# Performance work log

Measured on AMD Instinct MI355X. Metric: run time of the kernel, lower is better.

## Reference

```python
import jax, jax.numpy as jnp
import numpy as np

C = 256
NUM_HEADS = 4
NBLK = 6  # 3 stages x depth 2
WS = (2, 8, 8)   # 3D window
SS = (1, 4, 4)   # shift for odd blocks
N_WIN = WS[0] * WS[1] * WS[2]  # 128 tokens per window
RPB_SIZE = (2 * WS[0] - 1) * (2 * WS[1] - 1) * (2 * WS[2] - 1)  # 675


def _rel_index():
    coords = np.stack(np.meshgrid(np.arange(WS[0]), np.arange(WS[1]), np.arange(WS[2]), indexing='ij'))
    coords = coords.reshape(3, -1)
    rel = (coords[:, :, None] - coords[:, None, :]).transpose(1, 2, 0)
    rel[:, :, 0] += WS[0] - 1
    rel[:, :, 1] += WS[1] - 1
    rel[:, :, 2] += WS[2] - 1
    rel[:, :, 0] *= (2 * WS[1] - 1) * (2 * WS[2] - 1)
    rel[:, :, 1] *= (2 * WS[2] - 1)
    return jnp.asarray(rel.sum(-1))  # [N_WIN, N_WIN]

REL_IDX = _rel_index()


def window_partition(x):
    # [B,D,H,W,C] -> [B*nW, N_WIN, C]
    B, D, H, W, Cc = x.shape
    x = x.reshape(B, D // WS[0], WS[0], H // WS[1], WS[1], W // WS[2], WS[2], Cc)
    return x.transpose(0, 1, 3, 5, 2, 4, 6, 7).reshape(-1, N_WIN, Cc)


def window_reverse(win, B, D, H, W):
    Cc = win.shape[-1]
    x = win.reshape(B, D // WS[0], H // WS[1], W // WS[2], WS[0], WS[1], WS[2], Cc)
    return x.transpose(0, 1, 4, 2, 5, 3, 6, 7).reshape(B, D, H, W, Cc)


def attn_mask(D, H, W):
    # standard shifted-window mask, computed on host constants
    img = np.zeros((1, D, H, W, 1), np.float32)
    cnt = 0
    for d in (slice(0, -WS[0]), slice(-WS[0], -SS[0]), slice(-SS[0], None)):
        for h in (slice(0, -WS[1]), slice(-WS[1], -SS[1]), slice(-SS[1], None)):
            for w in (slice(0, -WS[2]), slice(-WS[2], -SS[2]), slice(-SS[2], None)):
                img[:, d, h, w, :] = cnt
                cnt += 1
    mw = img.reshape(1, D // WS[0], WS[0], H // WS[1], WS[1], W // WS[2], WS[2], 1)
    mw = mw.transpose(0, 1, 3, 5, 2, 4, 6, 7).reshape(-1, N_WIN)
    diff = mw[:, None, :] - mw[:, :, None]
    return jnp.asarray(np.where(diff != 0, -100.0, 0.0).astype(np.float32))  # [nW,N,N]


def layer_norm(x, g, b):
    mu = x.mean(-1, keepdims=True)
    var = ((x - mu) ** 2).mean(-1, keepdims=True)
    return (x - mu) * jax.lax.rsqrt(var + 1e-5) * g + b


def setup_inputs() -> dict:
    key = jax.random.key(0)
    ks = jax.random.split(key, 10)
    f = jax.random.normal
    s = 0.02
    return dict(
        x=f(ks[0], (2, 2, 2, 4096, C), jnp.float32),
        n1w=jnp.ones((NBLK, C), jnp.float32), n1b=jnp.zeros((NBLK, C), jnp.float32),
        qkv_w=f(ks[1], (NBLK, C, 3 * C), jnp.float32) * s, qkv_b=jnp.zeros((NBLK, 3 * C), jnp.float32),
        rpb=f(ks[2], (NBLK, RPB_SIZE, NUM_HEADS), jnp.float32) * s,
        proj_w=f(ks[3], (NBLK, C, C), jnp.float32) * s, proj_b=jnp.zeros((NBLK, C), jnp.float32),
        n2w=jnp.ones((NBLK, C), jnp.float32), n2b=jnp.zeros((NBLK, C), jnp.float32),
        mlp1_w=f(ks[4], (NBLK, C, 4 * C), jnp.float32) * s, mlp1_b=jnp.zeros((NBLK, 4 * C), jnp.float32),
        mlp2_w=f(ks[5], (NBLK, 4 * C, C), jnp.float32) * s, mlp2_b=jnp.zeros((NBLK, C), jnp.float32),
        exp_v_w=f(ks[6], (C, 2 * C), jnp.float32) * s,
        exp_v_nw=jnp.ones((C,), jnp.float32), exp_v_nb=jnp.zeros((C,), jnp.float32),
        exp_t_w=f(ks[7], (C, 2 * C), jnp.float32) * s,
        exp_t_nw=jnp.ones((C,), jnp.float32), exp_t_nb=jnp.zeros((C,), jnp.float32),
    )


def reference(x, n1w, n1b, qkv_w, qkv_b, rpb, proj_w, proj_b, n2w, n2b,
              mlp1_w, mlp1_b, mlp2_w, mlp2_b,
              exp_v_w, exp_v_nw, exp_v_nb, exp_t_w, exp_t_nw, exp_t_nb):
    B, T, V, L, _ = x.shape
    H = W = int(round(np.sqrt(L)))
    NH = NUM_HEADS
    dh = C // NH

    def block(h, i, D, shifted, mask):
        # h: [B, D, L, C]
        sc = h
        y = layer_norm(h, n1w[i], n1b[i]).reshape(B, D, H, W, C)
        if shifted:
            y = jnp.roll(y, (-SS[0], -SS[1], -SS[2]), axis=(1, 2, 3))
        win = window_partition(y)  # [B*nW, N, C]
        qkv = (win @ qkv_w[i] + qkv_b[i]).reshape(-1, N_WIN, 3, NH, dh)
        q, k, v = jnp.moveaxis(qkv, 2, 0)              # [B*nW, N, NH, dh]
        q = q.transpose(0, 2, 1, 3)
        k = k.transpose(0, 2, 1, 3)
        v = v.transpose(0, 2, 1, 3)                     # [B*nW, NH, N, dh]
        attn = jnp.einsum('whqd,whkd->whqk', q, k) * (dh ** -0.5)
        attn = attn + rpb[i][REL_IDX].transpose(2, 0, 1)[None]
        if mask is not None:
            nW = mask.shape[0]
            attn = attn.reshape(B, nW, NH, N_WIN, N_WIN) + mask[None, :, None]
            attn = attn.reshape(-1, NH, N_WIN, N_WIN)
        attn = jax.nn.softmax(attn, axis=-1)
        out = jnp.einsum('whqk,whkd->whqd', attn, v).transpose(0, 2, 1, 3).reshape(-1, N_WIN, C)
        out = out @ proj_w[i] + proj_b[i]
        y = window_reverse(out, B, D, H, W)
        if shifted:
            y = jnp.roll(y, (SS[0], SS[1], SS[2]), axis=(1, 2, 3))
        h = sc + y.reshape(B, D, L, C)
        z = layer_norm(h, n2w[i], n2b[i])
        z = jax.nn.gelu(z @ mlp1_w[i] + mlp1_b[i], approximate=False) @ mlp2_w[i] + mlp2_b[i]
        return h + z

    def stage(h, i0, D):
        mask = attn_mask(D, H, W)
        h = block(h, i0, D, False, None)
        h = block(h, i0 + 1, D, True, mask)
        return h

    # stage 1: swin over D = T*V
    h = x.reshape(B, T * V, L, C)
    h = stage(h, 0, T * V)
    h = h.reshape(B, T, V, L, C)

    # stage 2: view patch expand (V -> 2V) + swin
    h = (h @ exp_v_w).reshape(B, T, V, L, 2, C).transpose(0, 1, 2, 4, 3, 5).reshape(B, T, 2 * V, L, C)
    h = layer_norm(h, exp_v_nw, exp_v_nb)
    V2 = 2 * V
    h = h.reshape(B, T * V2, L, C)
    h = stage(h, 2, T * V2)
    h = h.reshape(B, T, V2, L, C)

    # stage 3: temporal patch expand (T -> 2T) + swin
    h = (h @ exp_t_w).reshape(B, T, V2, L, 2, C).transpose(0, 1, 4, 2, 3, 5).reshape(B, 2 * T, V2, L, C)
    h = layer_norm(h, exp_t_nw, exp_t_nb)
    T2 = 2 * T
    h = h.reshape(B, T2 * V2, L, C)
    h = stage(h, 4, T2 * V2)
    return h.reshape(B, T2, V2, L, C)
```

## Files before the change

### kernel.cpp

```cpp
#include <hip/hip_runtime.h>

typedef __bf16 bf16x8 __attribute__((ext_vector_type(8)));
typedef float f32x4 __attribute__((ext_vector_type(4)));
typedef unsigned short u16;
typedef unsigned int u32;

__device__ __forceinline__ u16 f2b(float f) {
    union { float f; u32 u; } v; v.f = f;
    u32 r = v.u + 0x7fffu + ((v.u >> 16) & 1u);
    return (u16)(r >> 16);
}
__device__ __forceinline__ float b2f(u16 u) {
    union { u32 u; float f; } v; v.u = ((u32)u) << 16; return v.f;
}
__device__ __forceinline__ void gl_lds16(const u16* g, u16* l) {
    __builtin_amdgcn_global_load_lds(
        (const __attribute__((address_space(1))) void*)g,
        (__attribute__((address_space(3))) void*)l, 16, 0, 0);
}

__global__ __launch_bounds__(256) void ln_kernel(
    const float* __restrict__ h, u16* __restrict__ out,
    const float* __restrict__ g, const float* __restrict__ bb,
    int D, int dsh, int shifted, int mode)
{
    const int lane = threadIdx.x & 63;
    const int t = blockIdx.x * 4 + (threadIdx.x >> 6);
    const float4 xv = *(const float4*)(h + (size_t)t * 256 + lane * 4);
    float s = xv.x + xv.y + xv.z + xv.w;
    float s2 = xv.x*xv.x + xv.y*xv.y + xv.z*xv.z + xv.w*xv.w;
    #pragma unroll
    for (int o = 32; o > 0; o >>= 1) { s += __shfl_xor(s, o); s2 += __shfl_xor(s2, o); }
    const float mu = s * 0.00390625f;
    const float var = s2 * 0.00390625f - mu * mu;
    const float rs = 1.0f / sqrtf(var + 1e-5f);
    const int c0 = lane * 4;
    const float4 gv = *(const float4*)(g + c0);
    const float4 bv = *(const float4*)(bb + c0);
    ushort4 o4;
    o4.x = f2b((xv.x - mu) * rs * gv.x + bv.x);
    o4.y = f2b((xv.y - mu) * rs * gv.y + bv.y);
    o4.z = f2b((xv.z - mu) * rs * gv.z + bv.z);
    o4.w = f2b((xv.w - mu) * rs * gv.w + bv.w);
    size_t oidx;
    if (mode == 1) {
        oidx = (size_t)t * 256 + c0;
    } else {
        const int b = t >> (dsh + 12);
        const int rem = t & ((1 << (dsh + 12)) - 1);
        int d = rem >> 12;
        const int l = rem & 4095;
        int hh = l >> 6, ww = l & 63;
        if (shifted) { d = d ? d - 1 : D - 1; hh = (hh - 4) & 63; ww = (ww - 4) & 63; }
        const int widx = (b << (dsh + 5)) + ((d >> 1) << 6) + ((hh >> 3) << 3) + (ww >> 3);
        const int n = ((d & 1) << 6) + ((hh & 7) << 3) + (ww & 7);
        oidx = ((size_t)(widx * 128 + n)) * 256 + c0;
    }
    *(ushort4*)(out + oidx) = o4;
}

__global__ __launch_bounds__(256) void cast_kernel(const float* __restrict__ in, u16* __restrict__ out, int n4)
{
    const int i = blockIdx.x * 256 + threadIdx.x;
    if (i >= n4) return;
    const float4 v = ((const float4*)in)[i];
    ushort4 o; o.x = f2b(v.x); o.y = f2b(v.y); o.z = f2b(v.z); o.w = f2b(v.w);
    ((ushort4*)out)[i] = o;
}

__global__ __launch_bounds__(256) void wt_kernel(const float* __restrict__ src, u16* __restrict__ dst, int K, int N)
{
    const size_t base = (size_t)blockIdx.y * K * N;
    const int idx = blockIdx.x * 256 + threadIdx.x;
    const int k = idx / N, n = idx - k * N;
    dst[base + (size_t)n * K + k] = f2b(src[base + idx]);
}

__global__ __launch_bounds__(256) void wt1f_kernel(const float* __restrict__ src, u16* __restrict__ dst)
{
    const size_t base = (size_t)blockIdx.y * 262144;
    const int t = blockIdx.x * 256 + threadIdx.x;
    const int e = t & 7, lane = (t >> 3) & 63, n = (t >> 9) & 3, kt = (t >> 11) & 7, c = t >> 14;
    const int k = kt * 32 + (lane >> 4) * 8 + e;
    const int mid = c * 64 + n * 16 + (lane & 15);
    dst[base + t] = f2b(src[base + (size_t)k * 1024 + mid]);
}

__global__ __launch_bounds__(256) void wt2f_kernel(const float* __restrict__ src, u16* __restrict__ dst)
{
    const size_t base = (size_t)blockIdx.y * 262144;
    const int t = blockIdx.x * 256 + threadIdx.x;
    const int e = t & 7, lane = (t >> 3) & 63, nt = (t >> 9) & 15, kt = (t >> 13) & 1, c = t >> 14;
    const int q = lane >> 4;
    const int mid = (2 * kt + (e >> 2)) * 16 + q * 4 + (e & 3);
    const int k = c * 64 + mid;
    const int out = nt * 16 + (lane & 15);
    dst[base + t] = f2b(src[base + (size_t)k * 256 + out]);
}

struct GemmP {
    const u16* A; const u16* Bt;
    int K;
    const float* bias;
    u16* outb;
    float* outf;
    const float* hin; float* hout;
    int D, shifted, nwsh, row_off;
};

template <int EPI>
__global__ __launch_bounds__(256, 2) void gemm_kernel(GemmP p)
{
    __shared__ __align__(16) char smem[33792];
    float* CF = (float*)smem;

    const int tid = threadIdx.x;
    const int m0 = blockIdx.x * 128, n0 = blockIdx.y * 128;
    const int K = p.K;
    const int lane = tid & 63;
    const int wv = tid >> 6;
    const int wm = (wv & 1) * 64, wn = (wv >> 1) * 64;
    const int l16 = lane & 15, quad = lane >> 4;

    f32x4 acc[4][4];
    #pragma unroll
    for (int a = 0; a < 4; a++)
        #pragma unroll
        for (int b = 0; b < 4; b++)
            acc[a][b] = f32x4{0.f, 0.f, 0.f, 0.f};

    const int lrow = lane >> 2;
    const int c16s = (lane & 3) ^ (lrow & 3);
    const int rA0 = wv * 16;
    const u16* Ag = p.A + (size_t)(m0 + rA0 + lrow) * K + c16s * 8;
    const u16* Bg = p.Bt + (size_t)(n0 + rA0 + lrow) * K + c16s * 8;
    const size_t j64 = (size_t)64 * K;
    const int fslot = (quad ^ (l16 & 3)) * 8;

    {
        u16* Al = (u16*)smem + rA0 * 32;
        u16* Bl = (u16*)(smem + 8192) + rA0 * 32;
        gl_lds16(Ag, Al);
        gl_lds16(Ag + j64, Al + 64 * 32);
        gl_lds16(Bg, Bl);
        gl_lds16(Bg + j64, Bl + 64 * 32);
    }
    __syncthreads();

    int kb = 0;
    for (int k0 = 0; k0 < K; k0 += 32, kb ^= 1) {
        if (k0 + 32 < K) {
            char* nb = smem + (kb ^ 1) * 16384;
            u16* Al = (u16*)nb + rA0 * 32;
            u16* Bl = (u16*)(nb + 8192) + rA0 * 32;
            gl_lds16(Ag + k0 + 32, Al);
            gl_lds16(Ag + j64 + k0 + 32, Al + 64 * 32);
            gl_lds16(Bg + k0 + 32, Bl);
            gl_lds16(Bg + j64 + k0 + 32, Bl + 64 * 32);
        }
        const u16* As = (const u16*)(smem + kb * 16384);
        const u16* Bs = (const u16*)(smem + kb * 16384 + 8192);
        bf16x8 af[4], bfr[4];
        #pragma unroll
        for (int mt = 0; mt < 4; mt++) af[mt] = *(const bf16x8*)(As + (wm + mt * 16 + l16) * 32 + fslot);
        #pragma unroll
        for (int nt = 0; nt < 4; nt++) bfr[nt] = *(const bf16x8*)(Bs + (wn + nt * 16 + l16) * 32 + fslot);
        #pragma unroll
        for (int mt = 0; mt < 4; mt++)
            #pragma unroll
            for (int nt = 0; nt < 4; nt++)
                acc[mt][nt] = __builtin_amdgcn_mfma_f32_16x16x32_bf16(af[mt], bfr[nt], acc[mt][nt], 0, 0, 0);
        __syncthreads();
    }

    const int crow = tid >> 2;
    const int p4 = (tid & 3) * 4;
    #pragma unroll
    for (int c = 0; c < 2; c++) {
        if (c) __syncthreads();
        if ((wv & 1) == c) {
            #pragma unroll
            for (int mt = 0; mt < 4; mt++)
                #pragma unroll
                for (int nt = 0; nt < 4; nt++)
                    #pragma unroll
                    for (int i = 0; i < 4; i++)
                        CF[(mt * 16 + quad * 4 + i) * 132 + wn + nt * 16 + l16] = acc[mt][nt][i];
        }
        __syncthreads();
        const int rowg = m0 + c * 64 + crow;
        size_t tokbase = 0;
        if constexpr (EPI == 1) {
            const int widx = rowg >> 7, n = rowg & 127;
            const int b = widx >> p.nwsh, rem = widx & ((1 << p.nwsh) - 1);
            int dd = ((rem >> 6) << 1) + (n >> 6);
            int hh = (((rem >> 3) & 7) << 3) + ((n >> 3) & 7);
            int ww = ((rem & 7) << 3) + (n & 7);
            if (p.shifted) { dd = (dd + 1 == p.D) ? 0 : dd + 1; hh = (hh + 4) & 63; ww = (ww + 4) & 63; }
            tokbase = ((size_t)((b * p.D + dd) * 4096 + hh * 64 + ww)) * 256;
        } else if constexpr (EPI == 3) {
            tokbase = (size_t)(p.row_off + rowg) * 256;
        }
        #pragma unroll
        for (int j = 0; j < 8; j++) {
            const int colf = j * 16 + p4;
            const int colg = n0 + colf;
            const float4 t = *(const float4*)(CF + crow * 132 + colf);
            const float4 bi = (EPI <= 3) ? *(const float4*)(p.bias + colg) : float4{0.f,0.f,0.f,0.f};
            if constexpr (EPI == 0) {
                const float sc = (colg < 256) ? 0.125f : 1.0f;
                ushort4 pk;
                pk.x = f2b((t.x + bi.x) * sc);
                pk.y = f2b((t.y + bi.y) * sc);
                pk.z = f2b((t.z + bi.z) * sc);
                pk.w = f2b((t.w + bi.w) * sc);
                *(ushort4*)(p.outb + (size_t)rowg * 768 + colg) = pk;
            } else if constexpr (EPI == 1 || EPI == 3) {
                const float* hi = p.hin + tokbase + colg;
                float* ho = p.hout + tokbase + colg;
                const float4 r = *(const float4*)hi;
                float4 o;
                o.x = r.x + t.x + bi.x;
                o.y = r.y + t.y + bi.y;
                o.z = r.z + t.z + bi.z;
                o.w = r.w + t.w + bi.w;
                *(float4*)ho = o;
            } else if constexpr (EPI == 2) {
                float4 g4;
                g4.x = t.x + bi.x; g4.y = t.y + bi.y; g4.z = t.z + bi.z; g4.w = t.w + bi.w;
                ushort4 pk;
                pk.x = f2b(0.5f * g4.x * (1.0f + erff(g4.x * 0.7071067811865475f)));
                pk.y = f2b(0.5f * g4.y * (1.0f + erff(g4.y * 0.7071067811865475f)));
                pk.z = f2b(0.5f * g4.z * (1.0f + erff(g4.z * 0.7071067811865475f)));
                pk.w = f2b(0.5f * g4.w * (1.0f + erff(g4.w * 0.7071067811865475f)));
                *(ushort4*)(p.outb + (size_t)rowg * 1024 + colg) = pk;
            } else {
                *(float4*)(p.outf + (size_t)rowg * 512 + colg) = t;
            }
        }
    }
}

struct MlpP {
    const u16* A;
    const u16* W1t;
    const u16* W2t;
    const float* b1;
    const float* b2;
    const float* hin;
    float* hout;
};

__global__ __launch_bounds__(512, 1) void mlp_fused_kernel(MlpP p)
{
    __shared__ __align__(16) char smem[131072];
    float* CF = (float*)smem;

    const int tid = threadIdx.x;
    const int lane = tid & 63;
    const int wv = tid >> 6;
    const int l16 = lane & 15, quad = lane >> 4;
    const int tok0 = blockIdx.x * 128;
    const int wtok = wv * 16;

    bf16x8 afr[8];
    #pragma unroll
    for (int kt = 0; kt < 8; kt++)
        afr[kt] = *(const bf16x8*)(p.A + (size_t)(tok0 + wtok + l16) * 256 + kt * 32 + quad * 8);

    f32x4 acc2[16];
    #pragma unroll
    for (int nt = 0; nt < 16; nt++) acc2[nt] = f32x4{0.f, 0.f, 0.f, 0.f};

    float b2v[16];
    #pragma unroll
    for (int nt = 0; nt < 16; nt++) b2v[nt] = p.b2[nt * 16 + l16];

    auto stage = [&](int c) {
        const u16* w1g = p.W1t + (size_t)c * 16384;
        const u16* w2g = p.W2t + (size_t)c * 16384;
        u16* w1b = (u16*)(smem + (c & 1) * 32768);
        u16* w2b = (u16*)(smem + 65536 + (c & 1) * 32768);
        #pragma unroll
        for (int f = 0; f < 4; f++) {
            const int fr = wv * 4 + f;
            gl_lds16(w1g + fr * 512 + lane * 8, w1b + fr * 512);
            gl_lds16(w2g + fr * 512 + lane * 8, w2b + fr * 512);
        }
    };

    stage(0);
    __syncthreads();

    #pragma unroll 2
    for (int c = 0; c < 16; c++) {
        if (c + 1 < 16) stage(c + 1);

        float b1v[4][4];
        #pragma unroll
        for (int n = 0; n < 4; n++)
            #pragma unroll
            for (int i = 0; i < 4; i++)
                b1v[n][i] = p.b1[c * 64 + n * 16 + quad * 4 + i];

        const u16* W1c = (const u16*)(smem + (c & 1) * 32768);
        f32x4 acc1[4];
        #pragma unroll
        for (int n = 0; n < 4; n++) acc1[n] = f32x4{0.f, 0.f, 0.f, 0.f};
        #pragma unroll
        for (int kt = 0; kt < 8; kt++) {
            bf16x8 w1f[4];
            #pragma unroll
            for (int n = 0; n < 4; n++)
                w1f[n] = *(const bf16x8*)(W1c + (kt * 4 + n) * 512 + lane * 8);
            #pragma unroll
            for (int n = 0; n < 4; n++)
                acc1[n] = __builtin_amdgcn_mfma_f32_16x16x32_bf16(w1f[n], afr[kt], acc1[n], 0, 0, 0);
        }

        bf16x8 pa0, pa1;
        #pragma unroll
        for (int n = 0; n < 4; n++) {
            #pragma unroll
            for (int i = 0; i < 4; i++) {
                const float x = acc1[n][i] + b1v[n][i];
                const float u = x * (1.0f + 0.044715f * x * x);
                const float em = __expf(-1.5957691216f * u);
                const float g = x * __builtin_amdgcn_rcpf(1.0f + em);
                if (n < 2) pa0[(n & 1) * 4 + i] = (__bf16)g;
                else       pa1[(n & 1) * 4 + i] = (__bf16)g;
            }
        }

        const u16* W2c = (const u16*)(smem + 65536 + (c & 1) * 32768);
        #pragma unroll
        for (int kt = 0; kt < 2; kt++) {
            const bf16x8 pk = kt ? pa1 : pa0;
            #pragma unroll
            for (int nt = 0; nt < 16; nt++) {
                const bf16x8 w2f = *(const bf16x8*)(W2c + (kt * 16 + nt) * 512 + lane * 8);
                acc2[nt] = __builtin_amdgcn_mfma_f32_16x16x32_bf16(pk, w2f, acc2[nt], 0, 0, 0);
            }
        }
        __syncthreads();
    }

    #pragma unroll
    for (int cc = 0; cc < 2; cc++) {
        __syncthreads();
        if ((wv >> 2) == cc) {
            const int rb = (wv & 3) * 16;
            #pragma unroll
            for (int nt = 0; nt < 16; nt++)
                #pragma unroll
                for (int i = 0; i < 4; i++)
                    CF[(rb + quad * 4 + i) * 260 + nt * 16 + l16] = acc2[nt][i] + b2v[nt];
        }
        __syncthreads();
        #pragma unroll
        for (int jj = 0; jj < 8; jj++) {
            const int idx = jj * 512 + tid;
            const int row = idx >> 6, c4 = (idx & 63) << 2;
            const size_t g = (size_t)(tok0 + cc * 64 + row) * 256 + c4;
            const float4 t = *(const float4*)(CF + row * 260 + c4);
            const float4 r = *(const float4*)(p.hin + g);
            float4 o;
            o.x = t.x + r.x; o.y = t.y + r.y; o.z = t.z + r.z; o.w = t.w + r.w;
            *(float4*)(p.hout + g) = o;
        }
    }
}

__global__ __launch_bounds__(256, 2) void attn_mfma_kernel(
    const u16* __restrict__ qkv, u16* __restrict__ att,
    const float* __restrict__ rpbp, int D, int shifted, int w0g, int nwsh)
{
    __shared__ __align__(16) char smem[57856];
    u16* Qs = (u16*)smem;
    u16* Ks = (u16*)(smem + 18432);
    u16* Ps = (u16*)smem;
    u16* Vt = (u16*)(smem + 36864);
    float* rb = (float*)(smem + 54272);
    int* lbl = (int*)(smem + 56972);

    const int wloc = blockIdx.x;
    const int head = blockIdx.y;
    const int tid = threadIdx.x;
    const u16* base = qkv + (size_t)wloc * 98304;

    #pragma unroll
    for (int it = 0; it < 4; it++) {
        const int id = it * 256 + tid;
        const int row = id >> 3, oct = id & 7;
        const size_t ro = (size_t)row * 768 + head * 64 + oct * 8;
        *(uint4*)(Qs + row * 72 + oct * 8) = *(const uint4*)(base + ro);
        *(uint4*)(Ks + row * 72 + oct * 8) = *(const uint4*)(base + ro + 256);
        uint4 vv = *(const uint4*)(base + ro + 512);
        const u16* vp = (const u16*)&vv;
        #pragma unroll
        for (int q = 0; q < 8; q++) Vt[(oct * 8 + q) * 136 + row] = vp[q];
    }
    for (int j = tid; j < 675; j += 256) rb[j] = rpbp[j * 4 + head];
    if (tid < 128) {
        int lv = 0;
        if (shifted) {
            const int widx = w0g + wloc;
            const int rem = widx & ((1 << nwsh) - 1);
            const int d0 = rem >> 6, h0 = (rem >> 3) & 7, w0 = rem & 7;
            const int wd = tid >> 6, wh = (tid >> 3) & 7, ww = tid & 7;
            const int rd = (d0 < (D >> 1) - 1) ? 0 : (1 + wd);
            const int rh = (h0 < 7) ? 0 : (1 + (wh >= 4));
            const int rw = (w0 < 7) ? 0 : (1 + (ww >= 4));
            lv = rd * 9 + rh * 3 + rw;
        }
        lbl[tid] = lv;
    }
    __syncthreads();

    const int wq = tid >> 6;
    const int lane = tid & 63;
    const int l16 = lane & 15, quad = lane >> 4;
    const int myrow0 = wq * 32;

    f32x4 sc[2][8];
    #pragma unroll
    for (int mt = 0; mt < 2; mt++)
        #pragma unroll
        for (int nt = 0; nt < 8; nt++)
            sc[mt][nt] = f32x4{0.f, 0.f, 0.f, 0.f};
    #pragma unroll
    for (int kt = 0; kt < 2; kt++) {
        bf16x8 aq[2];
        #pragma unroll
        for (int mt = 0; mt < 2; mt++)
            aq[mt] = *(const bf16x8*)(Qs + (myrow0 + mt * 16 + l16) * 72 + kt * 32 + quad * 8);
        bf16x8 bk[8];
        #pragma unroll
        for (int nt = 0; nt < 8; nt++)
            bk[nt] = *(const bf16x8*)(Ks + (nt * 16 + l16) * 72 + kt * 32 + quad * 8);
        #pragma unroll
        for (int mt = 0; mt < 2; mt++)
            #pragma unroll
            for (int nt = 0; nt < 8; nt++)
                sc[mt][nt] = __builtin_amdgcn_mfma_f32_16x16x32_bf16(aq[mt], bk[nt], sc[mt][nt], 0, 0, 0);
    }

    float linv[2][4];
    #pragma unroll
    for (int mt = 0; mt < 2; mt++) {
        #pragma unroll
        for (int i = 0; i < 4; i++) {
            const int row = myrow0 + mt * 16 + quad * 4 + i;
            const int rbase = ((row >> 6) + 1) * 225 + (((row >> 3) & 7) + 7) * 15 + ((row & 7) + 7);
            const int lq = lbl[row];
            float mx = -1e30f;
            float sv[8];
            #pragma unroll
            for (int nt = 0; nt < 8; nt++) {
                const int col = nt * 16 + l16;
                float v = sc[mt][nt][i] + rb[rbase - (col >> 6) * 225 - ((col >> 3) & 7) * 15 - (col & 7)];
                if (shifted && lq != lbl[col]) v -= 100.0f;
                sv[nt] = v;
                mx = fmaxf(mx, v);
            }
            #pragma unroll
            for (int o = 1; o < 16; o <<= 1) mx = fmaxf(mx, __shfl_xor(mx, o));
            float l = 0.0f;
            #pragma unroll
            for (int nt = 0; nt < 8; nt++) {
                const float pp = __expf(sv[nt] - mx);
                sc[mt][nt][i] = pp;
                l += pp;
            }
            #pragma unroll
            for (int o = 1; o < 16; o <<= 1) l += __shfl_xor(l, o);
            linv[mt][i] = 1.0f / l;
        }
    }

    __syncthreads();
    #pragma unroll
    for (int mt = 0; mt < 2; mt++)
        #pragma unroll
        for (int nt = 0; nt < 8; nt++)
            #pragma unroll
            for (int i = 0; i < 4; i++)
                Ps[(myrow0 + mt * 16 + quad * 4 + i) * 136 + nt * 16 + l16] = f2b(sc[mt][nt][i]);

    f32x4 oc[2][4];
    #pragma unroll
    for (int mt = 0; mt < 2; mt++)
        #pragma unroll
        for (int nt = 0; nt < 4; nt++)
            oc[mt][nt] = f32x4{0.f, 0.f, 0.f, 0.f};
    #pragma unroll
    for (int kt = 0; kt < 4; kt++) {
        bf16x8 ap[2];
        #pragma unroll
        for (int mt = 0; mt < 2; mt++)
            ap[mt] = *(const bf16x8*)(Ps + (myrow0 + mt * 16 + l16) * 136 + kt * 32 + quad * 8);
        bf16x8 bv[4];
        #pragma unroll
        for (int nt = 0; nt < 4; nt++)
            bv[nt] = *(const bf16x8*)(Vt + (nt * 16 + l16) * 136 + kt * 32 + quad * 8);
        #pragma unroll
        for (int mt = 0; mt < 2; mt++)
            #pragma unroll
            for (int nt = 0; nt < 4; nt++)
                oc[mt][nt] = __builtin_amdgcn_mfma_f32_16x16x32_bf16(ap[mt], bv[nt], oc[mt][nt], 0, 0, 0);
    }

    #pragma unroll
    for (int mt = 0; mt < 2; mt++)
        #pragma unroll
        for (int nt = 0; nt < 4; nt++)
            #pragma unroll
            for (int i = 0; i < 4; i++) {
                const int row = myrow0 + mt * 16 + quad * 4 + i;
                const int col = nt * 16 + l16;
                att[(size_t)(wloc * 128 + row) * 256 + head * 64 + col] = f2b(oc[mt][nt][i] * linv[mt][i]);
            }
}

__global__ __launch_bounds__(256) void expand_ln_kernel(
    const float* __restrict__ sc, float* __restrict__ hout,
    const float* __restrict__ g, const float* __restrict__ bb,
    int it0, int typ)
{
    const int lane = threadIdx.x & 63;
    const int ot = blockIdx.x * 4 + (threadIdx.x >> 6);
    const int itl = ot >> 1, e = ot & 1;
    const float4 xv = *(const float4*)(sc + (size_t)itl * 512 + e * 256 + lane * 4);
    float s = xv.x + xv.y + xv.z + xv.w;
    float s2 = xv.x*xv.x + xv.y*xv.y + xv.z*xv.z + xv.w*xv.w;
    #pragma unroll
    for (int o = 32; o > 0; o >>= 1) { s += __shfl_xor(s, o); s2 += __shfl_xor(s2, o); }
    const float mu = s * 0.00390625f;
    const float var = s2 * 0.00390625f - mu * mu;
    const float rs = 1.0f / sqrtf(var + 1e-5f);
    const int c0 = lane * 4;
    const float4 gv = *(const float4*)(g + c0);
    const float4 bv = *(const float4*)(bb + c0);
    float4 y;
    y.x = (xv.x - mu) * rs * gv.x + bv.x;
    y.y = (xv.y - mu) * rs * gv.y + bv.y;
    y.z = (xv.z - mu) * rs * gv.z + bv.z;
    y.w = (xv.w - mu) * rs * gv.w + bv.w;
    const int it = it0 + itl;
    size_t otg;
    if (typ == 0) {
        const int b = it >> 14, rr = it & 16383;
        const int t = rr >> 13, v = (rr >> 12) & 1, l = rr & 4095;
        otg = (size_t)(((b * 2 + t) * 4 + v * 2 + e) * 4096 + l);
    } else {
        const int b = it >> 15, rr = it & 32767;
        const int t = rr >> 14, v2 = (rr >> 12) & 3, l = rr & 4095;
        otg = (size_t)(((b * 4 + t * 2 + e) * 4 + v2) * 4096 + l);
    }
    *(float4*)(hout + otg * 256 + c0) = y;
}

extern "C" void kernel_launch(void* const* d_in, const int* in_sizes, int n_in,
                              void* d_out, int out_size, void* d_ws, size_t ws_size,
                              hipStream_t stream)
{
    const float* x      = (const float*)d_in[0];
    const float* n1w    = (const float*)d_in[1];
    const float* n1b    = (const float*)d_in[2];
    const float* qkv_w  = (const float*)d_in[3];
    const float* qkv_b  = (const float*)d_in[4];
    const float* rpb    = (const float*)d_in[5];
    const float* proj_w = (const float*)d_in[6];
    const float* proj_b = (const float*)d_in[7];
    const float* n2w    = (const float*)d_in[8];
    const float* n2b    = (const float*)d_in[9];
    const float* mlp1_w = (const float*)d_in[10];
    const float* mlp1_b = (const float*)d_in[11];
    const float* mlp2_w = (const float*)d_in[12];
    const float* mlp2_b = (const float*)d_in[13];
    const float* expv_w = (const float*)d_in[14];
    const float* expv_nw= (const float*)d_in[15];
    const float* expv_nb= (const float*)d_in[16];
    const float* expt_w = (const float*)d_in[17];
    const float* expt_nw= (const float*)d_in[18];
    const float* expt_nb= (const float*)d_in[19];
    (void)in_sizes; (void)n_in; (void)out_size;

    if (ws_size < 352321536ULL) return;

    char* ws = (char*)d_ws;
    float* h    = (float*)ws;
    u16*  winb  = (u16*)(ws + 134217728LL);
    u16*  att   = (u16*)(ws + 134217728LL + 67108864LL);
    char* scr   = ws + 134217728LL + 2LL * 67108864LL;
    u16*  scrb  = (u16*)scr;
    float* scrf = (float*)scr;
    u16* qkvT   = (u16*)(ws + 134217728LL + 3LL * 67108864LL);
    u16* projT  = qkvT + 6 * 768 * 256;
    u16* mlp1T  = projT + 6 * 256 * 256;
    u16* mlp2T  = mlp1T + 6 * 1024 * 256;
    u16* expvT  = mlp2T + 6 * 256 * 1024;
    u16* exptT  = expvT + 512 * 256;

    wt_kernel<<<dim3(768, 6), 256, 0, stream>>>(qkv_w, qkvT, 256, 768);
    wt_kernel<<<dim3(256, 6), 256, 0, stream>>>(proj_w, projT, 256, 256);
    wt1f_kernel<<<dim3(1024, 6), 256, 0, stream>>>(mlp1_w, mlp1T);
    wt2f_kernel<<<dim3(1024, 6), 256, 0, stream>>>(mlp2_w, mlp2T);
    wt_kernel<<<dim3(512, 1), 256, 0, stream>>>(expv_w, expvT, 256, 512);
    wt_kernel<<<dim3(512, 1), 256, 0, stream>>>(expt_w, exptT, 256, 512);
    hipMemcpyAsync(h, x, 33554432ULL, hipMemcpyDeviceToDevice, stream);

    for (int s = 0; s < 3; s++) {
        const int D = 4 << s;
        const int dsh = 2 + s;
        const int nwsh = dsh + 5;
        const int tokens = 2 * D * 4096;
        const int nch = tokens / 32768;
        for (int j = 0; j < 2; j++) {
            const int i = 2 * s + j;
            ln_kernel<<<dim3(tokens / 4), 256, 0, stream>>>(h, winb, n1w + i * 256, n1b + i * 256, D, dsh, j, 0);
            for (int c = 0; c < nch; c++) {
                GemmP gq{};
                gq.A = winb + (size_t)c * 32768 * 256;
                gq.Bt = qkvT + (size_t)i * 768 * 256;
                gq.K = 256; gq.bias = qkv_b + i * 768; gq.outb = scrb;
                gemm_kernel<0><<<dim3(256, 6), 256, 0, stream>>>(gq);
                attn_mfma_kernel<<<dim3(256, 4), 256, 0, stream>>>(scrb, att + (size_t)c * 32768 * 256,
                                                                   rpb + i * 675 * 4, D, j, c * 256, nwsh);
            }
            GemmP gp{};
            gp.A = att; gp.Bt = projT + (size_t)i * 256 * 256; gp.K = 256;
            gp.bias = proj_b + i * 256; gp.hin = h; gp.hout = h;
            gp.D = D; gp.shifted = j; gp.nwsh = nwsh;
            gemm_kernel<1><<<dim3(tokens / 128, 2), 256, 0, stream>>>(gp);
            ln_kernel<<<dim3(tokens / 4), 256, 0, stream>>>(h, winb, n2w + i * 256, n2b + i * 256, D, dsh, 0, 1);
            MlpP mp{};
            mp.A = winb;
            mp.W1t = mlp1T + (size_t)i * 262144;
            mp.W2t = mlp2T + (size_t)i * 262144;
            mp.b1 = mlp1_b + i * 1024;
            mp.b2 = mlp2_b + i * 256;
            mp.hin = h;
            mp.hout = (s == 2 && j == 1) ? (float*)d_out : h;
            mlp_fused_kernel<<<dim3(tokens / 128), 512, 0, stream>>>(mp);
        }
        if (s < 2) {
            const int ntok = tokens;
            cast_kernel<<<dim3(ntok * 64 / 256), 256, 0, stream>>>(h, winb, ntok * 64);
            const u16* eT = (s == 0) ? expvT : exptT;
            const float* eg = (s == 0) ? expv_nw : expt_nw;
            const float* eb = (s == 0) ? expv_nb : expt_nb;
            for (int c = 0; c < ntok / 32768; c++) {
                GemmP ge{};
                ge.A = winb + (size_t)c * 32768 * 256; ge.Bt = eT; ge.K = 256; ge.outf = scrf;
                gemm_kernel<4><<<dim3(256, 4), 256, 0, stream>>>(ge);
                expand_ln_kernel<<<dim3(16384), 256, 0, stream>>>(scrf, h, eg, eb, c * 32768, s);
            }
        }
    }
}
```

Before: 2.440 ms.

## Double tokens per wave in fused MLP kernel to reuse staged weights

Each wave in the fused MLP kernel now processes two 16-token row tiles (32 tokens) instead of one, so each block covers 256 tokens and the grid is halved. Every weight fragment read from LDS feeds two MFMAs, and each block's staged W1/W2 chunks serve twice as many tokens. This cuts per-token LDS weight reads and global weight traffic. In exchange, accumulator and register pressure roughly doubles and there are fewer blocks to spread across the CUs.

Result: slower. 2.601 ms (+6.6%).

```diff
diff --git a/kernel.cpp b/kernel.cpp
--- a/kernel.cpp
+++ b/kernel.cpp
@@ -260,21 +260,22 @@
     const int lane = tid & 63;
     const int wv = tid >> 6;
     const int l16 = lane & 15, quad = lane >> 4;
-    const int tok0 = blockIdx.x * 128;
-    const int wtok = wv * 16;
-
-    bf16x8 afr[8];
-    #pragma unroll
-    for (int kt = 0; kt < 8; kt++)
-        afr[kt] = *(const bf16x8*)(p.A + (size_t)(tok0 + wtok + l16) * 256 + kt * 32 + quad * 8);
-
-    f32x4 acc2[16];
-    #pragma unroll
-    for (int nt = 0; nt < 16; nt++) acc2[nt] = f32x4{0.f, 0.f, 0.f, 0.f};
-
-    float b2v[16];
-    #pragma unroll
-    for (int nt = 0; nt < 16; nt++) b2v[nt] = p.b2[nt * 16 + l16];
+    const int tok0 = blockIdx.x * 256;
+    const int wtok = wv * 32;
+
+    bf16x8 afr0[8], afr1[8];
+    #pragma unroll
+    for (int kt = 0; kt < 8; kt++) {
+        afr0[kt] = *(const bf16x8*)(p.A + (size_t)(tok0 + wtok + l16) * 256 + kt * 32 + quad * 8);
+        afr1[kt] = *(const bf16x8*)(p.A + (size_t)(tok0 + wtok + 16 + l16) * 256 + kt * 32 + quad * 8);
+    }
+
+    f32x4 acc2a[16], acc2b[16];
+    #pragma unroll
+    for (int nt = 0; nt < 16; nt++) {
+        acc2a[nt] = f32x4{0.f, 0.f, 0.f, 0.f};
+        acc2b[nt] = f32x4{0.f, 0.f, 0.f, 0.f};
+    }
 
     auto stage = [&](int c) {
         const u16* w1g = p.W1t + (size_t)c * 16384;
@@ -304,9 +305,12 @@
                 b1v[n][i] = p.b1[c * 64 + n * 16 + quad * 4 + i];
 
         const u16* W1c = (const u16*)(smem + (c & 1) * 32768);
-        f32x4 acc1[4];
-        #pragma unroll
-        for (int n = 0; n < 4; n++) acc1[n] = f32x4{0.f, 0.f, 0.f, 0.f};
+        f32x4 acc1a[4], acc1b[4];
+        #pragma unroll
+        for (int n = 0; n < 4; n++) {
+            acc1a[n] = f32x4{0.f, 0.f, 0.f, 0.f};
+            acc1b[n] = f32x4{0.f, 0.f, 0.f, 0.f};
+        }
         #pragma unroll
         for (int kt = 0; kt < 8; kt++) {
             bf16x8 w1f[4];
@@ -314,47 +318,67 @@
             for (int n = 0; n < 4; n++)
                 w1f[n] = *(const bf16x8*)(W1c + (kt * 4 + n) * 512 + lane * 8);
             #pragma unroll
-            for (int n = 0; n < 4; n++)
-                acc1[n] = __builtin_amdgcn_mfma_f32_16x16x32_bf16(w1f[n], afr[kt], acc1[n], 0, 0, 0);
-        }
-
-        bf16x8 pa0, pa1;
+            for (int n = 0; n < 4; n++) {
+                acc1a[n] = __builtin_amdgcn_mfma_f32_16x16x32_bf16(w1f[n], afr0[kt], acc1a[n], 0, 0, 0);
+                acc1b[n] = __builtin_amdgcn_mfma_f32_16x16x32_bf16(w1f[n], afr1[kt], acc1b[n], 0, 0, 0);
+            }
+        }
+
+        bf16x8 pa0a, pa1a, pa0b, pa1b;
         #pragma unroll
         for (int n = 0; n < 4; n++) {
             #pragma unroll
             for (int i = 0; i < 4; i++) {
-                const float x = acc1[n][i] + b1v[n][i];
-                const float u = x * (1.0f + 0.044715f * x * x);
-                const float em = __expf(-1.5957691216f * u);
-                const float g = x * __builtin_amdgcn_rcpf(1.0f + em);
-                if (n < 2) pa0[(n & 1) * 4 + i] = (__bf16)g;
-                else       pa1[(n & 1) * 4 + i] = (__bf16)g;
+                {
+                    const float x = acc1a[n][i] + b1v[n][i];
+                    const float u = x * (1.0f + 0.044715f * x * x);
+                    const float em = __expf(-1.5957691216f * u);
+                    const float g = x * __builtin_amdgcn_rcpf(1.0f + em);
+                    if (n < 2) pa0a[(n & 1) * 4 + i] = (__bf16)g;
+                    else       pa1a[(n & 1) * 4 + i] = (__bf16)g;
+                }
+                {
+                    const float x = acc1b[n][i] + b1v[n][i];
+                    const float u = x * (1.0f + 0.044715f * x * x);
+                    const float em = __expf(-1.5957691216f * u);
+                    const float g = x * __builtin_amdgcn_rcpf(1.0f + em);
+                    if (n < 2) pa0b[(n & 1) * 4 + i] = (__bf16)g;
+                    else       pa1b[(n & 1) * 4 + i] = (__bf16)g;
+                }
             }
         }
 
         const u16* W2c = (const u16*)(smem + 65536 + (c & 1) * 32768);
         #pragma unroll
         for (int kt = 0; kt < 2; kt++) {
-            const bf16x8 pk = kt ? pa1 : pa0;
+            const bf16x8 pka = kt ? pa1a : pa0a;
+            const bf16x8 pkb = kt ? pa1b : pa0b;
             #pragma unroll
             for (int nt = 0; nt < 16; nt++) {
                 const bf16x8 w2f = *(const bf16x8*)(W2c + (kt * 16 + nt) * 512 + lane * 8);
-                acc2[nt] = __builtin_amdgcn_mfma_f32_16x16x32_bf16(pk, w2f, acc2[nt], 0, 0, 0);
+                acc2a[nt] = __builtin_amdgcn_mfma_f32_16x16x32_bf16(pka, w2f, acc2a[nt], 0, 0, 0);
+                acc2b[nt] = __builtin_amdgcn_mfma_f32_16x16x32_bf16(pkb, w2f, acc2b[nt], 0, 0, 0);
             }
         }
         __syncthreads();
     }
 
-    #pragma unroll
-    for (int cc = 0; cc < 2; cc++) {
+    float b2v[16];
+    #pragma unroll
+    for (int nt = 0; nt < 16; nt++) b2v[nt] = p.b2[nt * 16 + l16];
+
+    #pragma unroll
+    for (int cc = 0; cc < 4; cc++) {
         __syncthreads();
-        if ((wv >> 2) == cc) {
-            const int rb = (wv & 3) * 16;
+        if ((wv >> 1) == cc) {
+            const int rb = (wv & 1) * 32;
             #pragma unroll
             for (int nt = 0; nt < 16; nt++)
                 #pragma unroll
-                for (int i = 0; i < 4; i++)
-                    CF[(rb + quad * 4 + i) * 260 + nt * 16 + l16] = acc2[nt][i] + b2v[nt];
+                for (int i = 0; i < 4; i++) {
+                    CF[(rb + quad * 4 + i) * 260 + nt * 16 + l16] = acc2a[nt][i] + b2v[nt];
+                    CF[(rb + 16 + quad * 4 + i) * 260 + nt * 16 + l16] = acc2b[nt][i] + b2v[nt];
+                }
         }
         __syncthreads();
         #pragma unroll
@@ -642,7 +666,7 @@
             mp.b2 = mlp2_b + i * 256;
             mp.hin = h;
             mp.hout = (s == 2 && j == 1) ? (float*)d_out : h;
-            mlp_fused_kernel<<<dim3(tokens / 128), 512, 0, stream>>>(mp);
+            mlp_fused_kernel<<<dim3(tokens / 256), 512, 0, stream>>>(mp);
         }
         if (s < 2) {
             const int ntok = tokens;
```

## Split MLP waves into 2x2 token/hidden tiles with LDS exchange of GELU activations

Applied to the files above, without the earlier changes.

Each pair of waves now covers 32 tokens, and each wave in the pair handles half of the hidden chunk and half of the output columns. Every W1/W2 fragment read from LDS is therefore reused across two token groups, roughly halving per-wave LDS weight traffic. GELU activations are swapped through a new 16KB LDS area behind an extra barrier in each chunk. In exchange the kernel uses more LDS (144KB), adds a barrier per iteration, and drops the unroll-by-2.

Result: no change. 2.447 ms (+0.3%).

```diff
diff --git a/kernel.cpp b/kernel.cpp
--- a/kernel.cpp
+++ b/kernel.cpp
@@ -253,28 +253,30 @@
 
 __global__ __launch_bounds__(512, 1) void mlp_fused_kernel(MlpP p)
 {
-    __shared__ __align__(16) char smem[131072];
+    __shared__ __align__(16) char smem[147456];
     float* CF = (float*)smem;
+    u16* ex = (u16*)(smem + 131072);
 
     const int tid = threadIdx.x;
     const int lane = tid & 63;
     const int wv = tid >> 6;
+    const int tg = wv >> 1, oh = wv & 1;
     const int l16 = lane & 15, quad = lane >> 4;
     const int tok0 = blockIdx.x * 128;
-    const int wtok = wv * 16;
-
-    bf16x8 afr[8];
-    #pragma unroll
-    for (int kt = 0; kt < 8; kt++)
-        afr[kt] = *(const bf16x8*)(p.A + (size_t)(tok0 + wtok + l16) * 256 + kt * 32 + quad * 8);
-
-    f32x4 acc2[16];
-    #pragma unroll
-    for (int nt = 0; nt < 16; nt++) acc2[nt] = f32x4{0.f, 0.f, 0.f, 0.f};
-
-    float b2v[16];
-    #pragma unroll
-    for (int nt = 0; nt < 16; nt++) b2v[nt] = p.b2[nt * 16 + l16];
+
+    bf16x8 afr[2][8];
+    #pragma unroll
+    for (int g = 0; g < 2; g++)
+        #pragma unroll
+        for (int kt = 0; kt < 8; kt++)
+            afr[g][kt] = *(const bf16x8*)(p.A + (size_t)(tok0 + tg * 32 + g * 16 + l16) * 256 + kt * 32 + quad * 8);
+
+    f32x4 acc2[2][8];
+    #pragma unroll
+    for (int g = 0; g < 2; g++)
+        #pragma unroll
+        for (int nt = 0; nt < 8; nt++)
+            acc2[g][nt] = f32x4{0.f, 0.f, 0.f, 0.f};
 
     auto stage = [&](int c) {
         const u16* w1g = p.W1t + (size_t)c * 16384;
@@ -292,69 +294,90 @@
     stage(0);
     __syncthreads();
 
-    #pragma unroll 2
     for (int c = 0; c < 16; c++) {
         if (c + 1 < 16) stage(c + 1);
 
-        float b1v[4][4];
-        #pragma unroll
-        for (int n = 0; n < 4; n++)
-            #pragma unroll
-            for (int i = 0; i < 4; i++)
-                b1v[n][i] = p.b1[c * 64 + n * 16 + quad * 4 + i];
-
         const u16* W1c = (const u16*)(smem + (c & 1) * 32768);
-        f32x4 acc1[4];
-        #pragma unroll
-        for (int n = 0; n < 4; n++) acc1[n] = f32x4{0.f, 0.f, 0.f, 0.f};
+        f32x4 acc1[2][2];
+        #pragma unroll
+        for (int g = 0; g < 2; g++)
+            #pragma unroll
+            for (int n = 0; n < 2; n++)
+                acc1[g][n] = f32x4{0.f, 0.f, 0.f, 0.f};
         #pragma unroll
         for (int kt = 0; kt < 8; kt++) {
-            bf16x8 w1f[4];
-            #pragma unroll
-            for (int n = 0; n < 4; n++)
-                w1f[n] = *(const bf16x8*)(W1c + (kt * 4 + n) * 512 + lane * 8);
-            #pragma unroll
-            for (int n = 0; n < 4; n++)
-                acc1[n] = __builtin_amdgcn_mfma_f32_16x16x32_bf16(w1f[n], afr[kt], acc1[n], 0, 0, 0);
-        }
-
-        bf16x8 pa0, pa1;
-        #pragma unroll
-        for (int n = 0; n < 4; n++) {
+            bf16x8 w1f[2];
+            #pragma unroll
+            for (int n = 0; n < 2; n++)
+                w1f[n] = *(const bf16x8*)(W1c + (kt * 4 + oh * 2 + n) * 512 + lane * 8);
+            #pragma unroll
+            for (int g = 0; g < 2; g++)
+                #pragma unroll
+                for (int n = 0; n < 2; n++)
+                    acc1[g][n] = __builtin_amdgcn_mfma_f32_16x16x32_bf16(w1f[n], afr[g][kt], acc1[g][n], 0, 0, 0);
+        }
+
+        bf16x8 pa[2];
+        #pragma unroll
+        for (int n = 0; n < 2; n++) {
+            const float4 b1q = *(const float4*)(p.b1 + c * 64 + oh * 32 + n * 16 + quad * 4);
             #pragma unroll
             for (int i = 0; i < 4; i++) {
-                const float x = acc1[n][i] + b1v[n][i];
-                const float u = x * (1.0f + 0.044715f * x * x);
-                const float em = __expf(-1.5957691216f * u);
-                const float g = x * __builtin_amdgcn_rcpf(1.0f + em);
-                if (n < 2) pa0[(n & 1) * 4 + i] = (__bf16)g;
-                else       pa1[(n & 1) * 4 + i] = (__bf16)g;
-            }
-        }
+                const float b1i = (i == 0) ? b1q.x : (i == 1) ? b1q.y : (i == 2) ? b1q.z : b1q.w;
+                #pragma unroll
+                for (int g = 0; g < 2; g++) {
+                    const float x = acc1[g][n][i] + b1i;
+                    const float u = x * (1.0f + 0.044715f * x * x);
+                    const float em = __expf(-1.5957691216f * u);
+                    const float gv = x * __builtin_amdgcn_rcpf(1.0f + em);
+                    pa[g][n * 4 + i] = (__bf16)gv;
+                }
+            }
+        }
+
+        #pragma unroll
+        for (int g = 0; g < 2; g++)
+            *(bf16x8*)(ex + ((tg * 2 + g) * 2 + oh) * 512 + lane * 8) = pa[g];
+        asm volatile("s_waitcnt lgkmcnt(0)\ns_barrier" ::: "memory");
 
         const u16* W2c = (const u16*)(smem + 65536 + (c & 1) * 32768);
         #pragma unroll
         for (int kt = 0; kt < 2; kt++) {
-            const bf16x8 pk = kt ? pa1 : pa0;
-            #pragma unroll
-            for (int nt = 0; nt < 16; nt++) {
-                const bf16x8 w2f = *(const bf16x8*)(W2c + (kt * 16 + nt) * 512 + lane * 8);
-                acc2[nt] = __builtin_amdgcn_mfma_f32_16x16x32_bf16(pk, w2f, acc2[nt], 0, 0, 0);
+            bf16x8 a2[2];
+            if (kt == oh) {
+                a2[0] = pa[0]; a2[1] = pa[1];
+            } else {
+                #pragma unroll
+                for (int g = 0; g < 2; g++)
+                    a2[g] = *(const bf16x8*)(ex + ((tg * 2 + g) * 2 + (1 - oh)) * 512 + lane * 8);
+            }
+            #pragma unroll
+            for (int nt = 0; nt < 8; nt++) {
+                const bf16x8 w2f = *(const bf16x8*)(W2c + (kt * 16 + oh * 8 + nt) * 512 + lane * 8);
+                #pragma unroll
+                for (int g = 0; g < 2; g++)
+                    acc2[g][nt] = __builtin_amdgcn_mfma_f32_16x16x32_bf16(a2[g], w2f, acc2[g][nt], 0, 0, 0);
             }
         }
         __syncthreads();
     }
+
+    float b2v[8];
+    #pragma unroll
+    for (int nt = 0; nt < 8; nt++) b2v[nt] = p.b2[oh * 128 + nt * 16 + l16];
 
     #pragma unroll
     for (int cc = 0; cc < 2; cc++) {
         __syncthreads();
         if ((wv >> 2) == cc) {
-            const int rb = (wv & 3) * 16;
-            #pragma unroll
-            for (int nt = 0; nt < 16; nt++)
+            const int rb = (tg & 1) * 32;
+            #pragma unroll
+            for (int g = 0; g < 2; g++)
                 #pragma unroll
-                for (int i = 0; i < 4; i++)
-                    CF[(rb + quad * 4 + i) * 260 + nt * 16 + l16] = acc2[nt][i] + b2v[nt];
+                for (int nt = 0; nt < 8; nt++)
+                    #pragma unroll
+                    for (int i = 0; i < 4; i++)
+                        CF[(rb + g * 16 + quad * 4 + i) * 260 + oh * 128 + nt * 16 + l16] = acc2[g][nt][i] + b2v[nt];
         }
         __syncthreads();
         #pragma unroll
```

## Halve MLP hidden chunk size to shrink LDS and registers for occupancy

Applied to the files above, without the earlier changes.

The fused MLP kernel now streams the 1024-wide hidden dimension in 32 chunks of 32 instead of 16 chunks of 64. The weight pre-packing kernels change to match the new fragment order. Double-buffered LDS drops from 128KB to 72KB and fewer accumulators and bias registers stay live, with launch bounds raised to allow more blocks per CU. The cost is twice as many barriers and loop iterations, each with less MFMA work to hide load latency.

Result: no change. 2.413 ms (median of 3 runs) (-1.1%).

```diff
diff --git a/kernel.cpp b/kernel.cpp
--- a/kernel.cpp
+++ b/kernel.cpp
@@ -80,9 +80,9 @@
 {
     const size_t base = (size_t)blockIdx.y * 262144;
     const int t = blockIdx.x * 256 + threadIdx.x;
-    const int e = t & 7, lane = (t >> 3) & 63, n = (t >> 9) & 3, kt = (t >> 11) & 7, c = t >> 14;
+    const int e = t & 7, lane = (t >> 3) & 63, n2 = (t >> 9) & 1, kt = (t >> 10) & 7, c = t >> 13;
     const int k = kt * 32 + (lane >> 4) * 8 + e;
-    const int mid = c * 64 + n * 16 + (lane & 15);
+    const int mid = c * 32 + n2 * 16 + (lane & 15);
     dst[base + t] = f2b(src[base + (size_t)k * 1024 + mid]);
 }
 
@@ -90,10 +90,10 @@
 {
     const size_t base = (size_t)blockIdx.y * 262144;
     const int t = blockIdx.x * 256 + threadIdx.x;
-    const int e = t & 7, lane = (t >> 3) & 63, nt = (t >> 9) & 15, kt = (t >> 13) & 1, c = t >> 14;
+    const int e = t & 7, lane = (t >> 3) & 63, nt = (t >> 9) & 15, c = t >> 13;
     const int q = lane >> 4;
-    const int mid = (2 * kt + (e >> 2)) * 16 + q * 4 + (e & 3);
-    const int k = c * 64 + mid;
+    const int mid = (e >> 2) * 16 + q * 4 + (e & 3);
+    const int k = c * 32 + mid;
     const int out = nt * 16 + (lane & 15);
     dst[base + t] = f2b(src[base + (size_t)k * 256 + out]);
 }
@@ -251,9 +251,9 @@
     float* hout;
 };
 
-__global__ __launch_bounds__(512, 1) void mlp_fused_kernel(MlpP p)
-{
-    __shared__ __align__(16) char smem[131072];
+__global__ __launch_bounds__(512, 4) void mlp_fused_kernel(MlpP p)
+{
+    __shared__ __align__(16) char smem[73728];
     float* CF = (float*)smem;
 
     const int tid = threadIdx.x;
@@ -272,18 +272,14 @@
     #pragma unroll
     for (int nt = 0; nt < 16; nt++) acc2[nt] = f32x4{0.f, 0.f, 0.f, 0.f};
 
-    float b2v[16];
-    #pragma unroll
-    for (int nt = 0; nt < 16; nt++) b2v[nt] = p.b2[nt * 16 + l16];
-
     auto stage = [&](int c) {
-        const u16* w1g = p.W1t + (size_t)c * 16384;
-        const u16* w2g = p.W2t + (size_t)c * 16384;
-        u16* w1b = (u16*)(smem + (c & 1) * 32768);
-        u16* w2b = (u16*)(smem + 65536 + (c & 1) * 32768);
-        #pragma unroll
-        for (int f = 0; f < 4; f++) {
-            const int fr = wv * 4 + f;
+        const u16* w1g = p.W1t + (size_t)c * 8192;
+        const u16* w2g = p.W2t + (size_t)c * 8192;
+        u16* w1b = (u16*)(smem + (c & 1) * 16384);
+        u16* w2b = (u16*)(smem + 32768 + (c & 1) * 16384);
+        #pragma unroll
+        for (int f = 0; f < 2; f++) {
+            const int fr = wv * 2 + f;
             gl_lds16(w1g + fr * 512 + lane * 8, w1b + fr * 512);
             gl_lds16(w2g + fr * 512 + lane * 8, w2b + fr * 512);
         }
@@ -292,58 +288,51 @@
     stage(0);
     __syncthreads();
 
-    #pragma unroll 2
-    for (int c = 0; c < 16; c++) {
-        if (c + 1 < 16) stage(c + 1);
-
-        float b1v[4][4];
-        #pragma unroll
-        for (int n = 0; n < 4; n++)
-            #pragma unroll
-            for (int i = 0; i < 4; i++)
-                b1v[n][i] = p.b1[c * 64 + n * 16 + quad * 4 + i];
-
-        const u16* W1c = (const u16*)(smem + (c & 1) * 32768);
-        f32x4 acc1[4];
-        #pragma unroll
-        for (int n = 0; n < 4; n++) acc1[n] = f32x4{0.f, 0.f, 0.f, 0.f};
+    for (int c = 0; c < 32; c++) {
+        if (c + 1 < 32) stage(c + 1);
+
+        const u16* W1c = (const u16*)(smem + (c & 1) * 16384);
+        f32x4 acc1[2];
+        acc1[0] = f32x4{0.f, 0.f, 0.f, 0.f};
+        acc1[1] = f32x4{0.f, 0.f, 0.f, 0.f};
         #pragma unroll
         for (int kt = 0; kt < 8; kt++) {
-            bf16x8 w1f[4];
-            #pragma unroll
-            for (int n = 0; n < 4; n++)
-                w1f[n] = *(const bf16x8*)(W1c + (kt * 4 + n) * 512 + lane * 8);
-            #pragma unroll
-            for (int n = 0; n < 4; n++)
-                acc1[n] = __builtin_amdgcn_mfma_f32_16x16x32_bf16(w1f[n], afr[kt], acc1[n], 0, 0, 0);
-        }
-
-        bf16x8 pa0, pa1;
-        #pragma unroll
-        for (int n = 0; n < 4; n++) {
+            bf16x8 w1f[2];
+            #pragma unroll
+            for (int n2 = 0; n2 < 2; n2++)
+                w1f[n2] = *(const bf16x8*)(W1c + (kt * 2 + n2) * 512 + lane * 8);
+            #pragma unroll
+            for (int n2 = 0; n2 < 2; n2++)
+                acc1[n2] = __builtin_amdgcn_mfma_f32_16x16x32_bf16(w1f[n2], afr[kt], acc1[n2], 0, 0, 0);
+        }
+
+        bf16x8 pa;
+        #pragma unroll
+        for (int n2 = 0; n2 < 2; n2++) {
+            const float4 b1q = *(const float4*)(p.b1 + c * 32 + n2 * 16 + quad * 4);
             #pragma unroll
             for (int i = 0; i < 4; i++) {
-                const float x = acc1[n][i] + b1v[n][i];
+                const float b1i = (i == 0) ? b1q.x : (i == 1) ? b1q.y : (i == 2) ? b1q.z : b1q.w;
+                const float x = acc1[n2][i] + b1i;
                 const float u = x * (1.0f + 0.044715f * x * x);
                 const float em = __expf(-1.5957691216f * u);
                 const float g = x * __builtin_amdgcn_rcpf(1.0f + em);
-                if (n < 2) pa0[(n & 1) * 4 + i] = (__bf16)g;
-                else       pa1[(n & 1) * 4 + i] = (__bf16)g;
+                pa[n2 * 4 + i] = (__bf16)g;
             }
         }
 
-        const u16* W2c = (const u16*)(smem + 65536 + (c & 1) * 32768);
-        #pragma unroll
-        for (int kt = 0; kt < 2; kt++) {
-            const bf16x8 pk = kt ? pa1 : pa0;
-            #pragma unroll
-            for (int nt = 0; nt < 16; nt++) {
-                const bf16x8 w2f = *(const bf16x8*)(W2c + (kt * 16 + nt) * 512 + lane * 8);
-                acc2[nt] = __builtin_amdgcn_mfma_f32_16x16x32_bf16(pk, w2f, acc2[nt], 0, 0, 0);
-            }
+        const u16* W2c = (const u16*)(smem + 32768 + (c & 1) * 16384);
+        #pragma unroll
+        for (int nt = 0; nt < 16; nt++) {
+            const bf16x8 w2f = *(const bf16x8*)(W2c + nt * 512 + lane * 8);
+            acc2[nt] = __builtin_amdgcn_mfma_f32_16x16x32_bf16(pa, w2f, acc2[nt], 0, 0, 0);
         }
         __syncthreads();
     }
+
+    float b2v[16];
+    #pragma unroll
+    for (int nt = 0; nt < 16; nt++) b2v[nt] = p.b2[nt * 16 + l16];
 
     #pragma unroll
     for (int cc = 0; cc < 2; cc++) {
```
